# Kernel tuning notes

Measured on AMD Instinct MI355X. Metric: run time of the kernel, lower is better.

The kernel has to match this reference:

```python
import jax, jax.numpy as jnp
import numpy as np

F = 256   # num_features
H = 64    # num_hidden_features
B = 8192  # batch


def setup_inputs() -> dict:
    key = jax.random.key(0)
    ks = jax.random.split(key, 7)
    s1 = 1.0  # torch Linear init scale ~ U(-1/sqrt(fan_in), ...); use normal*1/sqrt(fan_in)
    sH = 1.0 / np.sqrt(H)
    x = jax.random.normal(ks[0], (B, F), dtype=jnp.float32)
    # Stacked per-feature weights. torch Linear: y = x @ W.T + b, W:[out,in].
    w1 = jax.random.normal(ks[1], (F, H), dtype=jnp.float32) * s1      # [F, H]  (in=1)
    b1 = jax.random.normal(ks[2], (F, H), dtype=jnp.float32) * s1
    w2 = jax.random.normal(ks[3], (F, H, H), dtype=jnp.float32) * sH   # [F, out, in]
    b2 = jax.random.normal(ks[4], (F, H), dtype=jnp.float32) * sH
    w3 = jax.random.normal(ks[5], (F, H), dtype=jnp.float32) * sH      # [F, H] (out=1)
    b3 = jax.random.normal(ks[6], (F,), dtype=jnp.float32) * sH
    return {"x": x, "w1": w1, "b1": b1, "w2": w2, "b2": b2, "w3": w3, "b3": b3}


def reference(x, w1, b1, w2, b2, w3, b3):
    # x: [B, F]; per-feature MLP 1 -> H -> H -> 1, fused via batched einsums.
    h1 = jax.nn.relu(x[:, :, None] * w1[None, :, :] + b1[None])        # [B, F, H]
    h2 = jax.nn.relu(jnp.einsum('bfh,foh->bfo', h1, w2) + b2[None])    # [B, F, H]
    out = jnp.einsum('bfh,fh->bf', h2, w3) + b3[None]                  # [B, F]
    return out
```

## Files before the change

### kernel.cpp

```cpp
#include <hip/hip_runtime.h>
#include <hip/hip_bf16.h>


namespace {

constexpr int kF = 256;
constexpr int kH = 64;
constexpr int kB = 8192;

constexpr int kFPB     = 4;
constexpr int kRPB     = 128;
constexpr int kThreads = 256;
constexpr int kFG      = kF / kFPB;
constexpr int kRG      = kB / kRPB;
constexpr int kBlocks  = kFG * kRG;
constexpr int kPasses  = kRPB / 16;
constexpr int kXP      = 10;

using f32x2  = __attribute__((ext_vector_type(2))) float;
using f32x4  = __attribute__((ext_vector_type(4))) float;
using bf16x4 = __attribute__((ext_vector_type(4))) __bf16;
using bf16x8 = __attribute__((ext_vector_type(8))) __bf16;

__global__ __launch_bounds__(256)
void pack_w2(const float* __restrict__ w2, __bf16* __restrict__ w2p)
{
  const int wid  = (int)threadIdx.x >> 6;
  const int lane = (int)threadIdx.x & 63;
  const int f    = (int)blockIdx.x * 4 + wid;
  const int l15  = lane & 15;
  const int lg   = lane >> 4;

  const float* w2f = w2 + (size_t)f * (kH * kH);
  #pragma unroll
  for (int t = 0; t < 4; ++t) {
    const int o = t * 16 + l15;
    #pragma unroll
    for (int ks = 0; ks < 2; ++ks) {
      const float* p = w2f + o * kH + ks * 32 + lg * 8;
      const f32x4 lo = *reinterpret_cast<const f32x4*>(p);
      const f32x4 hi = *reinterpret_cast<const f32x4*>(p + 4);
      const bf16x8 v = __builtin_shufflevector(
          __builtin_convertvector(lo, bf16x4),
          __builtin_convertvector(hi, bf16x4), 0, 1, 2, 3, 4, 5, 6, 7);
      *reinterpret_cast<bf16x8*>(
          w2p + (((size_t)f * 8 + t * 2 + ks) * 64 + lane) * 8) = v;
    }
  }
}

__global__ __launch_bounds__(kThreads, 3)
void mlp_pf_v9(const float* __restrict__ x,
               const float* __restrict__ w1,
               const float* __restrict__ b1,
               const __bf16* __restrict__ w2p,
               const float* __restrict__ b2,
               const float* __restrict__ w3,
               const float* __restrict__ b3,
               float* __restrict__ out)
{
  __shared__ float xs[kFPB][16][kXP];
  __shared__ float outb[kRPB][kFPB + 1];

  const int tid  = (int)threadIdx.x;
  const int wid  = tid >> 6;
  const int lane = tid & 63;
  const int l15  = lane & 15;
  const int lg   = lane >> 4;

  const int fg = (int)blockIdx.x & (kFG - 1);
  const int rg = (int)blockIdx.x >> 6;
  const int f  = fg * kFPB + wid;
  const int r0 = rg * kRPB;

  bf16x8 w2frag[4][2];
  {
    const __bf16* base = w2p + ((size_t)f * 8 * 64 + lane) * 8;
    #pragma unroll
    for (int t = 0; t < 4; ++t)
      #pragma unroll
      for (int ks = 0; ks < 2; ++ks)
        w2frag[t][ks] = *reinterpret_cast<const bf16x8*>(
            base + (size_t)(t * 2 + ks) * 64 * 8);
  }

  if (tid < kRPB) {
    const int rr = tid;
    const f32x4 v = *reinterpret_cast<const f32x4*>(
        x + (size_t)(r0 + rr) * kF + fg * kFPB);
    const int a = rr & 15, b = rr >> 4;
    xs[0][a][b] = v[0]; xs[1][a][b] = v[1];
    xs[2][a][b] = v[2]; xs[3][a][b] = v[3];
  }

  f32x4 w1v[2][2], b1v[2][2];
  #pragma unroll
  for (int ks = 0; ks < 2; ++ks) {
    const float* pw = w1 + f * kH + ks * 32 + lg * 8;
    const float* pb = b1 + f * kH + ks * 32 + lg * 8;
    w1v[ks][0] = *reinterpret_cast<const f32x4*>(pw);
    w1v[ks][1] = *reinterpret_cast<const f32x4*>(pw + 4);
    b1v[ks][0] = *reinterpret_cast<const f32x4*>(pb);
    b1v[ks][1] = *reinterpret_cast<const f32x4*>(pb + 4);
  }
  f32x4 b2c[4], w3v[4];
  #pragma unroll
  for (int t = 0; t < 4; ++t) {
    b2c[t] = *reinterpret_cast<const f32x4*>(b2 + f * kH + t * 16 + lg * 4);
    w3v[t] = *reinterpret_cast<const f32x4*>(w3 + f * kH + t * 16 + lg * 4);
  }
  const float b3v = b3[f];

  __syncthreads();

  const f32x4 zero4 = {0.f, 0.f, 0.f, 0.f};
  float keep = 0.f;

  #pragma unroll
  for (int pp = 0; pp < kPasses / 2; ++pp) {
    const f32x2 xp = *reinterpret_cast<const f32x2*>(&xs[wid][l15][2 * pp]);

    bf16x8 h1A[2], h1B[2];
    #pragma unroll
    for (int ks = 0; ks < 2; ++ks) {
      f32x4 aA = w1v[ks][0] * xp[0] + b1v[ks][0];
      f32x4 bA = w1v[ks][1] * xp[0] + b1v[ks][1];
      f32x4 aB = w1v[ks][0] * xp[1] + b1v[ks][0];
      f32x4 bB = w1v[ks][1] * xp[1] + b1v[ks][1];
      aA = __builtin_elementwise_max(aA, zero4);
      bA = __builtin_elementwise_max(bA, zero4);
      aB = __builtin_elementwise_max(aB, zero4);
      bB = __builtin_elementwise_max(bB, zero4);
      h1A[ks] = __builtin_shufflevector(
          __builtin_convertvector(aA, bf16x4),
          __builtin_convertvector(bA, bf16x4), 0, 1, 2, 3, 4, 5, 6, 7);
      h1B[ks] = __builtin_shufflevector(
          __builtin_convertvector(aB, bf16x4),
          __builtin_convertvector(bB, bf16x4), 0, 1, 2, 3, 4, 5, 6, 7);
    }

    f32x4 p4A = zero4, p4B = zero4;
    #pragma unroll
    for (int t = 0; t < 4; ++t) {
      f32x4 accA = __builtin_amdgcn_mfma_f32_16x16x32_bf16(
          w2frag[t][0], h1A[0], b2c[t], 0, 0, 0);
      f32x4 accB = __builtin_amdgcn_mfma_f32_16x16x32_bf16(
          w2frag[t][0], h1B[0], b2c[t], 0, 0, 0);
      accA = __builtin_amdgcn_mfma_f32_16x16x32_bf16(
          w2frag[t][1], h1A[1], accA, 0, 0, 0);
      accB = __builtin_amdgcn_mfma_f32_16x16x32_bf16(
          w2frag[t][1], h1B[1], accB, 0, 0, 0);
      const f32x4 rA = __builtin_elementwise_max(accA, zero4);
      const f32x4 rB = __builtin_elementwise_max(accB, zero4);
      p4A += rA * w3v[t];
      p4B += rB * w3v[t];
    }

    float sA = (p4A[0] + p4A[1]) + (p4A[2] + p4A[3]);
    float sB = (p4B[0] + p4B[1]) + (p4B[2] + p4B[3]);
    sA += __shfl_xor(sA, 16);
    sB += __shfl_xor(sB, 16);
    sA += __shfl_xor(sA, 32);
    sB += __shfl_xor(sB, 32);

    const int pA = 2 * pp, pB = 2 * pp + 1;
    keep = (lg == (pA & 3)) ? sA : keep;
    keep = (lg == (pB & 3)) ? sB : keep;
    if ((pB & 3) == 3) {
      outb[(pB >> 2) * 64 + lane][wid] = keep + b3v;
    }
  }

  __syncthreads();

  if (tid < kRPB) {
    const int rr = tid;
    const f32x4 v = {outb[rr][0], outb[rr][1], outb[rr][2], outb[rr][3]};
    *reinterpret_cast<f32x4*>(out + (size_t)(r0 + rr) * kF + fg * kFPB) = v;
  }
}

}

extern "C" void kernel_launch(void* const* d_in, const int* in_sizes, int n_in,
                              void* d_out, int out_size, void* d_ws, size_t ws_size,
                              hipStream_t stream) {
  const float* x  = (const float*)d_in[0];
  const float* w1 = (const float*)d_in[1];
  const float* b1 = (const float*)d_in[2];
  const float* w2 = (const float*)d_in[3];
  const float* b2 = (const float*)d_in[4];
  const float* w3 = (const float*)d_in[5];
  const float* b3 = (const float*)d_in[6];
  float* out = (float*)d_out;

  __bf16* w2p = (__bf16*)d_ws;

  hipLaunchKernelGGL(pack_w2, dim3(kF / 4), dim3(256), 0, stream, w2, w2p);
  hipLaunchKernelGGL(mlp_pf_v9, dim3(kBlocks), dim3(kThreads), 0, stream,
                     x, w1, b1, w2p, b2, w3, b3, out);
}
```

Measured before the change: 41.35 us.

## Compute layer-3 reduction with MFMA by permuting W2 output rows

The W2 rows and b2 are permuted in the pack kernel so that each lane's MFMA accumulator outputs form a valid bf16 B-operand fragment. This lets the final dot with w3 run as two more MFMA instructions instead of VALU multiply-adds plus cross-lane shuffle reductions, with b3 folded into the accumulator init. The trade-offs are that h2 and w3 are now rounded to bf16, which adds precision loss, and the pack kernel does extra work.

After: 40.37 us. -2.4%, faster.

```diff
diff --git a/kernel.cpp b/kernel.cpp
--- a/kernel.cpp
+++ b/kernel.cpp
@@ -23,7 +23,9 @@
 using bf16x8 = __attribute__((ext_vector_type(8))) __bf16;
 
 __global__ __launch_bounds__(256)
-void pack_w2(const float* __restrict__ w2, __bf16* __restrict__ w2p)
+void pack_params(const float* __restrict__ w2, const float* __restrict__ b2,
+                 const float* __restrict__ w3, __bf16* __restrict__ w2p,
+                 float* __restrict__ b2p, __bf16* __restrict__ w3p)
 {
   const int wid  = (int)threadIdx.x >> 6;
   const int lane = (int)threadIdx.x & 63;
@@ -34,10 +36,10 @@
   const float* w2f = w2 + (size_t)f * (kH * kH);
   #pragma unroll
   for (int t = 0; t < 4; ++t) {
-    const int o = t * 16 + l15;
+    const int o2 = 32 * (t >> 1) + 8 * (l15 >> 2) + 4 * (t & 1) + (l15 & 3);
     #pragma unroll
     for (int ks = 0; ks < 2; ++ks) {
-      const float* p = w2f + o * kH + ks * 32 + lg * 8;
+      const float* p = w2f + o2 * kH + ks * 32 + lg * 8;
       const f32x4 lo = *reinterpret_cast<const f32x4*>(p);
       const f32x4 hi = *reinterpret_cast<const f32x4*>(p + 4);
       const bf16x8 v = __builtin_shufflevector(
@@ -47,17 +49,24 @@
           w2p + (((size_t)f * 8 + t * 2 + ks) * 64 + lane) * 8) = v;
     }
   }
+
+  {
+    const int jt = lane >> 4, jlg = (lane >> 2) & 3, jr = lane & 3;
+    const int o  = 32 * (jt >> 1) + 8 * jlg + 4 * (jt & 1) + jr;
+    b2p[(size_t)f * kH + lane] = b2[(size_t)f * kH + o];
+  }
+  w3p[(size_t)f * kH + lane] = (__bf16)w3[(size_t)f * kH + lane];
 }
 
 __global__ __launch_bounds__(kThreads, 3)
-void mlp_pf_v9(const float* __restrict__ x,
-               const float* __restrict__ w1,
-               const float* __restrict__ b1,
-               const __bf16* __restrict__ w2p,
-               const float* __restrict__ b2,
-               const float* __restrict__ w3,
-               const float* __restrict__ b3,
-               float* __restrict__ out)
+void mlp_pf_v11(const float* __restrict__ x,
+                const float* __restrict__ w1,
+                const float* __restrict__ b1,
+                const __bf16* __restrict__ w2p,
+                const float* __restrict__ b2p,
+                const __bf16* __restrict__ w3p,
+                const float* __restrict__ b3,
+                float* __restrict__ out)
 {
   __shared__ float xs[kFPB][16][kXP];
   __shared__ float outb[kRPB][kFPB + 1];
@@ -103,13 +112,16 @@
     b1v[ks][0] = *reinterpret_cast<const f32x4*>(pb);
     b1v[ks][1] = *reinterpret_cast<const f32x4*>(pb + 4);
   }
-  f32x4 b2c[4], w3v[4];
-  #pragma unroll
-  for (int t = 0; t < 4; ++t) {
-    b2c[t] = *reinterpret_cast<const f32x4*>(b2 + f * kH + t * 16 + lg * 4);
-    w3v[t] = *reinterpret_cast<const f32x4*>(w3 + f * kH + t * 16 + lg * 4);
-  }
+  f32x4 b2c[4];
+  #pragma unroll
+  for (int t = 0; t < 4; ++t)
+    b2c[t] = *reinterpret_cast<const f32x4*>(b2p + f * kH + t * 16 + lg * 4);
+  bf16x8 w3f[2];
+  #pragma unroll
+  for (int ks = 0; ks < 2; ++ks)
+    w3f[ks] = *reinterpret_cast<const bf16x8*>(w3p + f * kH + ks * 32 + lg * 8);
   const float b3v = b3[f];
+  const f32x4 b3c = {b3v, b3v, b3v, b3v};
 
   __syncthreads();
 
@@ -139,35 +151,53 @@
           __builtin_convertvector(bB, bf16x4), 0, 1, 2, 3, 4, 5, 6, 7);
     }
 
-    f32x4 p4A = zero4, p4B = zero4;
+    f32x4 accA[4], accB[4];
     #pragma unroll
     for (int t = 0; t < 4; ++t) {
-      f32x4 accA = __builtin_amdgcn_mfma_f32_16x16x32_bf16(
+      accA[t] = __builtin_amdgcn_mfma_f32_16x16x32_bf16(
           w2frag[t][0], h1A[0], b2c[t], 0, 0, 0);
-      f32x4 accB = __builtin_amdgcn_mfma_f32_16x16x32_bf16(
+      accB[t] = __builtin_amdgcn_mfma_f32_16x16x32_bf16(
           w2frag[t][0], h1B[0], b2c[t], 0, 0, 0);
-      accA = __builtin_amdgcn_mfma_f32_16x16x32_bf16(
-          w2frag[t][1], h1A[1], accA, 0, 0, 0);
-      accB = __builtin_amdgcn_mfma_f32_16x16x32_bf16(
-          w2frag[t][1], h1B[1], accB, 0, 0, 0);
-      const f32x4 rA = __builtin_elementwise_max(accA, zero4);
-      const f32x4 rB = __builtin_elementwise_max(accB, zero4);
-      p4A += rA * w3v[t];
-      p4B += rB * w3v[t];
-    }
-
-    float sA = (p4A[0] + p4A[1]) + (p4A[2] + p4A[3]);
-    float sB = (p4B[0] + p4B[1]) + (p4B[2] + p4B[3]);
-    sA += __shfl_xor(sA, 16);
-    sB += __shfl_xor(sB, 16);
-    sA += __shfl_xor(sA, 32);
-    sB += __shfl_xor(sB, 32);
+      accA[t] = __builtin_amdgcn_mfma_f32_16x16x32_bf16(
+          w2frag[t][1], h1A[1], accA[t], 0, 0, 0);
+      accB[t] = __builtin_amdgcn_mfma_f32_16x16x32_bf16(
+          w2frag[t][1], h1B[1], accB[t], 0, 0, 0);
+    }
+
+    bf16x8 h2A0, h2A1, h2B0, h2B1;
+    {
+      const f32x4 rA0 = __builtin_elementwise_max(accA[0], zero4);
+      const f32x4 rA1 = __builtin_elementwise_max(accA[1], zero4);
+      const f32x4 rA2 = __builtin_elementwise_max(accA[2], zero4);
+      const f32x4 rA3 = __builtin_elementwise_max(accA[3], zero4);
+      const f32x4 rB0 = __builtin_elementwise_max(accB[0], zero4);
+      const f32x4 rB1 = __builtin_elementwise_max(accB[1], zero4);
+      const f32x4 rB2 = __builtin_elementwise_max(accB[2], zero4);
+      const f32x4 rB3 = __builtin_elementwise_max(accB[3], zero4);
+      h2A0 = __builtin_shufflevector(__builtin_convertvector(rA0, bf16x4),
+                                     __builtin_convertvector(rA1, bf16x4),
+                                     0, 1, 2, 3, 4, 5, 6, 7);
+      h2A1 = __builtin_shufflevector(__builtin_convertvector(rA2, bf16x4),
+                                     __builtin_convertvector(rA3, bf16x4),
+                                     0, 1, 2, 3, 4, 5, 6, 7);
+      h2B0 = __builtin_shufflevector(__builtin_convertvector(rB0, bf16x4),
+                                     __builtin_convertvector(rB1, bf16x4),
+                                     0, 1, 2, 3, 4, 5, 6, 7);
+      h2B1 = __builtin_shufflevector(__builtin_convertvector(rB2, bf16x4),
+                                     __builtin_convertvector(rB3, bf16x4),
+                                     0, 1, 2, 3, 4, 5, 6, 7);
+    }
+
+    f32x4 dA = __builtin_amdgcn_mfma_f32_16x16x32_bf16(w3f[0], h2A0, b3c, 0, 0, 0);
+    f32x4 dB = __builtin_amdgcn_mfma_f32_16x16x32_bf16(w3f[0], h2B0, b3c, 0, 0, 0);
+    dA = __builtin_amdgcn_mfma_f32_16x16x32_bf16(w3f[1], h2A1, dA, 0, 0, 0);
+    dB = __builtin_amdgcn_mfma_f32_16x16x32_bf16(w3f[1], h2B1, dB, 0, 0, 0);
 
     const int pA = 2 * pp, pB = 2 * pp + 1;
-    keep = (lg == (pA & 3)) ? sA : keep;
-    keep = (lg == (pB & 3)) ? sB : keep;
+    keep = (lg == (pA & 3)) ? dA[0] : keep;
+    keep = (lg == (pB & 3)) ? dB[0] : keep;
     if ((pB & 3) == 3) {
-      outb[(pB >> 2) * 64 + lane][wid] = keep + b3v;
+      outb[(pB >> 2) * 64 + lane][wid] = keep;
     }
   }
 
@@ -195,8 +225,11 @@
   float* out = (float*)d_out;
 
   __bf16* w2p = (__bf16*)d_ws;
-
-  hipLaunchKernelGGL(pack_w2, dim3(kF / 4), dim3(256), 0, stream, w2, w2p);
-  hipLaunchKernelGGL(mlp_pf_v9, dim3(kBlocks), dim3(kThreads), 0, stream,
-                     x, w1, b1, w2p, b2, w3, b3, out);
-}
+  float*  b2p = (float*)((char*)d_ws + (2u << 20));
+  __bf16* w3p = (__bf16*)((char*)d_ws + (2u << 20) + (64u << 10));
+
+  hipLaunchKernelGGL(pack_params, dim3(kF / 4), dim3(256), 0, stream,
+                     w2, b2, w3, w2p, b2p, w3p);
+  hipLaunchKernelGGL(mlp_pf_v11, dim3(kBlocks), dim3(kThreads), 0, stream,
+                     x, w1, b1, w2p, b2p, w3p, b3, out);
+}
```
